# Kernel optimization log

Measured on AMD Instinct MI355X. Metric: run time of the kernel, lower is better.

The kernel has to match this reference:

```python
import jax, jax.numpy as jnp
import numpy as np

D_MODEL, N_HEAD, D_FF = 768, 12, 3072
HEAD_DIM = D_MODEL // N_HEAD
EPS = 1e-5


def _layernorm(x, g, b):
    mu = jnp.mean(x, axis=-1, keepdims=True)
    var = jnp.mean((x - mu) ** 2, axis=-1, keepdims=True)
    return (x - mu) * jax.lax.rsqrt(var + EPS) * g + b


def setup_inputs() -> dict:
    key = jax.random.key(0)
    ks = jax.random.split(key, 14)
    s = 1.0 / np.sqrt(D_MODEL)
    sf = 1.0 / np.sqrt(D_FF)
    inp = {
        "x": jax.random.normal(ks[0], (2, 2048, D_MODEL), dtype=jnp.float32),
        "Wq": jax.random.normal(ks[1], (D_MODEL, D_MODEL), dtype=jnp.float32) * s,
        "bq": jnp.zeros((D_MODEL,), jnp.float32),
        "Wk": jax.random.normal(ks[2], (D_MODEL, D_MODEL), dtype=jnp.float32) * s,
        "bk": jnp.zeros((D_MODEL,), jnp.float32),
        "Wv": jax.random.normal(ks[3], (D_MODEL, D_MODEL), dtype=jnp.float32) * s,
        "bv": jnp.zeros((D_MODEL,), jnp.float32),
        "Wo": jax.random.normal(ks[4], (D_MODEL, D_MODEL), dtype=jnp.float32) * s,
        "bo": jnp.zeros((D_MODEL,), jnp.float32),
        "W1": jax.random.normal(ks[5], (D_MODEL, D_FF), dtype=jnp.float32) * s,
        "b1": jnp.zeros((D_FF,), jnp.float32),
        "W2": jax.random.normal(ks[6], (D_FF, D_MODEL), dtype=jnp.float32) * sf,
        "b2": jnp.zeros((D_MODEL,), jnp.float32),
        "ln1_g": jnp.ones((D_MODEL,), jnp.float32),
        "ln1_b": jnp.zeros((D_MODEL,), jnp.float32),
        "ln2_g": jnp.ones((D_MODEL,), jnp.float32),
        "ln2_b": jnp.zeros((D_MODEL,), jnp.float32),
    }
    return inp


def reference(x, Wq, bq, Wk, bk, Wv, bv, Wo, bo, W1, b1, W2, b2,
              ln1_g, ln1_b, ln2_g, ln2_b):
    B, S, D = x.shape
    # projections -> [B, H, S, hd]
    def proj(W, b):
        return (x @ W + b).reshape(B, S, N_HEAD, HEAD_DIM).transpose(0, 2, 1, 3)
    q, k, v = proj(Wq, bq), proj(Wk, bk), proj(Wv, bv)
    scores = jnp.einsum("bhqd,bhkd->bhqk", q, k) / jnp.sqrt(
        jnp.asarray(HEAD_DIM, jnp.float32))
    attn = jax.nn.softmax(scores, axis=-1)
    ctx = jnp.einsum("bhqk,bhkd->bhqd", attn, v)
    ctx = ctx.transpose(0, 2, 1, 3).reshape(B, S, D)
    attn_out = ctx @ Wo + bo
    h = _layernorm(x + attn_out, ln1_g, ln1_b)
    ffn = jax.nn.gelu(h @ W1 + b1, approximate=False) @ W2 + b2
    return _layernorm(h + ffn, ln2_g, ln2_b)
```

## Files before the change

### kernel.cpp

```cpp
#include <hip/hip_runtime.h>
#include <hip/hip_bf16.h>
#include <cstdint>
#include <cstddef>

typedef unsigned short u16;
typedef __bf16 bf16x8 __attribute__((ext_vector_type(8)));
typedef float f32x4 __attribute__((ext_vector_type(4)));

#define MFMA_BF16(a, b, c) __builtin_amdgcn_mfma_f32_16x16x32_bf16((a), (b), (c), 0, 0, 0)

#define GLDS16(g, l)                                                        \
  __builtin_amdgcn_global_load_lds(                                         \
      (__attribute__((address_space(1))) void*)(void*)(g),                  \
      (__attribute__((address_space(3))) void*)(void*)(l), 16, 0, 0)

#define QSCALE 0.18033688011112042f

__device__ __forceinline__ u16 f2bf(float x) {
  union { float f; unsigned u; } c; c.f = x;
  unsigned u = c.u;
  unsigned r = (u + 0x7fffu + ((u >> 16) & 1u)) >> 16;
  return (u16)r;
}


__global__ __launch_bounds__(256) void transpose_bf16_k(
    const float* __restrict__ in, u16* __restrict__ out, int K, int N) {
  __shared__ float tile[32][33];
  const int tx = threadIdx.x & 31, ty = threadIdx.x >> 5;
  const int bx = blockIdx.x * 32;
  const int by = blockIdx.y * 32;
#pragma unroll
  for (int j = 0; j < 32; j += 8)
    tile[ty + j][tx] = in[(size_t)(by + ty + j) * N + bx + tx];
  __syncthreads();
#pragma unroll
  for (int j = 0; j < 32; j += 8)
    out[(size_t)(bx + ty + j) * K + by + tx] = f2bf(tile[tx][ty + j]);
}

__global__ __launch_bounds__(256) void cvt_bf16_k(
    const float* __restrict__ in, u16* __restrict__ out, int n) {
  int i = (blockIdx.x * 256 + threadIdx.x) * 4;
  if (i + 3 < n) {
    const float4 v = *(const float4*)(in + i);
    ushort4 o;
    o.x = f2bf(v.x); o.y = f2bf(v.y); o.z = f2bf(v.z); o.w = f2bf(v.w);
    *(ushort4*)(out + i) = o;
  }
}

__global__ __launch_bounds__(256) void concat3_k(
    const float* __restrict__ a, const float* __restrict__ b,
    const float* __restrict__ c, float* __restrict__ out) {
  int i = blockIdx.x * 256 + threadIdx.x;
  if (i < 768) out[i] = a[i];
  else if (i < 1536) out[i] = b[i - 768];
  else if (i < 2304) out[i] = c[i - 1536];
}

template <int EPI>
__global__ __launch_bounds__(256) void gemm_bt(
    const u16* __restrict__ A, const u16* __restrict__ BT,
    const float* __restrict__ bias, int M, int N, int K,
    float* __restrict__ outf, u16* __restrict__ outb,
    u16* __restrict__ qo, u16* __restrict__ ko, u16* __restrict__ vto) {
  __shared__ __align__(16) u16 lsA[128 * 32];
  __shared__ __align__(16) u16 lsB[128 * 32];
  const int tid = threadIdx.x;
  const int w = tid >> 6, lane = tid & 63;
  const int wm = w & 1, wn = w >> 1;
  const int lrow = lane & 15, quad = lane >> 4;
  const int m0 = blockIdx.y * 128, n0 = blockIdx.x * 128;

  f32x4 acc[4][4];
#pragma unroll
  for (int i = 0; i < 4; ++i)
#pragma unroll
    for (int j = 0; j < 4; ++j) acc[i][j] = (f32x4){0.f, 0.f, 0.f, 0.f};

  const int off = tid * 16;
  const int srow = off >> 6;
  const int scol = (off & 63) >> 1;

  for (int k0 = 0; k0 < K; k0 += 32) {
    const u16* ga = A + (size_t)(m0 + srow) * K + k0 + scol;
    const u16* gb = BT + (size_t)(n0 + srow) * K + k0 + scol;
    GLDS16(ga, (char*)lsA + off);
    GLDS16(ga + (size_t)64 * K, (char*)lsA + 4096 + off);
    GLDS16(gb, (char*)lsB + off);
    GLDS16(gb + (size_t)64 * K, (char*)lsB + 4096 + off);
    __syncthreads();
    bf16x8 af[4], bfr[4];
#pragma unroll
    for (int ms = 0; ms < 4; ++ms)
      af[ms] = *(const bf16x8*)&lsA[(wm * 64 + ms * 16 + lrow) * 32 + quad * 8];
#pragma unroll
    for (int ns = 0; ns < 4; ++ns)
      bfr[ns] = *(const bf16x8*)&lsB[(wn * 64 + ns * 16 + lrow) * 32 + quad * 8];
#pragma unroll
    for (int ms = 0; ms < 4; ++ms)
#pragma unroll
      for (int ns = 0; ns < 4; ++ns)
        acc[ms][ns] = MFMA_BF16(af[ms], bfr[ns], acc[ms][ns]);
    __syncthreads();
  }

#pragma unroll
  for (int ms = 0; ms < 4; ++ms) {
    const int rbase = m0 + wm * 64 + ms * 16 + quad * 4;
#pragma unroll
    for (int ns = 0; ns < 4; ++ns) {
      const int col = n0 + wn * 64 + ns * 16 + lrow;
      const float bcol = bias[col];
      if constexpr (EPI == 1) {
#pragma unroll
        for (int r = 0; r < 4; ++r)
          outf[(size_t)(rbase + r) * N + col] = acc[ms][ns][r] + bcol;
      } else if constexpr (EPI == 2) {
#pragma unroll
        for (int r = 0; r < 4; ++r) {
          float v = acc[ms][ns][r] + bcol;
          float g = 0.5f * v * (1.0f + erff(v * 0.7071067811865476f));
          outb[(size_t)(rbase + r) * N + col] = f2bf(g);
        }
      } else {
        const int which = col / 768;
        const int rem = col - which * 768;
        const int hh = rem >> 6, dd = rem & 63;
        const int bI = rbase >> 11, sI = rbase & 2047;
        const size_t bh = (size_t)bI * 12 + hh;
        if (which == 0) {
#pragma unroll
          for (int r = 0; r < 4; ++r)
            qo[(bh * 2048 + sI + r) * 64 + dd] = f2bf((acc[ms][ns][r] + bcol) * QSCALE);
        } else if (which == 1) {
#pragma unroll
          for (int r = 0; r < 4; ++r)
            ko[(bh * 2048 + sI + r) * 64 + dd] = f2bf(acc[ms][ns][r] + bcol);
        } else {
          ushort4 pk;
          pk.x = f2bf(acc[ms][ns][0] + bcol);
          pk.y = f2bf(acc[ms][ns][1] + bcol);
          pk.z = f2bf(acc[ms][ns][2] + bcol);
          pk.w = f2bf(acc[ms][ns][3] + bcol);
          *(ushort4*)(vto + (bh * 64 + dd) * 2048 + sI) = pk;
        }
      }
    }
  }
}

__global__ __launch_bounds__(256) void attn_kernel(
    const u16* __restrict__ q, const u16* __restrict__ k,
    const u16* __restrict__ vT, u16* __restrict__ ctx) {
  __shared__ __align__(16) u16 lsK[64 * 64];
  __shared__ __align__(16) u16 lsV[64 * 64];
  __shared__ __align__(16) u16 lsP[4][16 * 64];
  const int tid = threadIdx.x;
  const int w = tid >> 6, lane = tid & 63;
  const int lrow = lane & 15, quad = lane >> 4;
  const int bh = blockIdx.y;
  const int b = bh / 12, h = bh - b * 12;
  const int q0 = blockIdx.x * 64;

  const u16* qbase = q + (size_t)bh * 2048 * 64;
  const u16* kbase = k + (size_t)bh * 2048 * 64;
  const u16* vbase = vT + (size_t)bh * 64 * 2048;

  const int qrow = q0 + w * 16 + lrow;
  const bf16x8 qf0 = *(const bf16x8*)(qbase + (size_t)qrow * 64 + quad * 8);
  const bf16x8 qf1 = *(const bf16x8*)(qbase + (size_t)qrow * 64 + 32 + quad * 8);

  float lsum[4] = {0.f, 0.f, 0.f, 0.f};
  f32x4 oacc[4];
#pragma unroll
  for (int d = 0; d < 4; ++d) oacc[d] = (f32x4){0.f, 0.f, 0.f, 0.f};

  const int off = tid * 16;
  const int srow = off >> 7;
  const int schunk = (off >> 4) & 7;
  const int sxc = schunk ^ (srow & 7);
  const int ksrc = srow * 64 + sxc * 8;
  const int vsrc0 = srow * 2048 + sxc * 8;

  const int c0 = quad ^ (lrow & 7);
  const int rd0 = c0 * 8, rd1 = (c0 ^ 4) * 8;

  u16* const lsPw = &lsP[w][0];
  const int jhi_base = lrow >> 3, jlo = lrow & 7;

  for (int kt = 0; kt < 2048; kt += 64) {
    GLDS16(kbase + (size_t)kt * 64 + ksrc, (char*)lsK + off);
    GLDS16(kbase + (size_t)(kt + 32) * 64 + ksrc, (char*)lsK + 4096 + off);
    GLDS16(vbase + vsrc0 + kt, (char*)lsV + off);
    GLDS16(vbase + vsrc0 + kt + 32 * 2048, (char*)lsV + 4096 + off);
    __syncthreads();

    f32x4 sc[4];
#pragma unroll
    for (int ns = 0; ns < 4; ++ns) {
      sc[ns] = (f32x4){0.f, 0.f, 0.f, 0.f};
      const u16* kr = &lsK[(ns * 16 + lrow) * 64];
      bf16x8 kf0 = *(const bf16x8*)(kr + rd0);
      bf16x8 kf1 = *(const bf16x8*)(kr + rd1);
      sc[ns] = MFMA_BF16(qf0, kf0, sc[ns]);
      sc[ns] = MFMA_BF16(qf1, kf1, sc[ns]);
    }

#pragma unroll
    for (int ns = 0; ns < 4; ++ns) {
      const int jhi = ns * 2 + jhi_base;
#pragma unroll
      for (int r = 0; r < 4; ++r) {
        float p = __builtin_amdgcn_exp2f(sc[ns][r]);
        lsum[r] += p;
        union { float f; unsigned u; } cv; cv.f = p;
        const int m = quad * 4 + r;
        lsPw[m * 64 + ((jhi ^ (m & 7)) * 8) + jlo] = (u16)(cv.u >> 16);
      }
    }

    const u16* pr = lsPw + lrow * 64;
    const bf16x8 pf0 = *(const bf16x8*)(pr + rd0);
    const bf16x8 pf1 = *(const bf16x8*)(pr + rd1);
#pragma unroll
    for (int d = 0; d < 4; ++d) {
      const u16* vr = &lsV[(d * 16 + lrow) * 64];
      bf16x8 vf0 = *(const bf16x8*)(vr + rd0);
      bf16x8 vf1 = *(const bf16x8*)(vr + rd1);
      oacc[d] = MFMA_BF16(pf0, vf0, oacc[d]);
      oacc[d] = MFMA_BF16(pf1, vf1, oacc[d]);
    }
    __syncthreads();
  }

#pragma unroll
  for (int r = 0; r < 4; ++r) {
#pragma unroll
    for (int mm = 1; mm <= 8; mm <<= 1) lsum[r] += __shfl_xor(lsum[r], mm);
  }
  float invl[4];
#pragma unroll
  for (int r = 0; r < 4; ++r) invl[r] = 1.f / lsum[r];

  const int srow_out = q0 + w * 16 + quad * 4;
#pragma unroll
  for (int d = 0; d < 4; ++d)
#pragma unroll
    for (int r = 0; r < 4; ++r)
      ctx[(size_t)(b * 2048 + srow_out + r) * 768 + h * 64 + d * 16 + lrow] =
          f2bf(oacc[d][r] * invl[r]);
}

__global__ __launch_bounds__(256) void ln_kernel(
    const float* __restrict__ a, const float* __restrict__ res,
    const float* __restrict__ g, const float* __restrict__ bb,
    float* __restrict__ outf, u16* __restrict__ outb) {
  const int row = blockIdx.x;
  const int tid = threadIdx.x;
  const float* pa = a + (size_t)row * 768;
  const float* pr = res + (size_t)row * 768;
  float v[3], s = 0.f, s2 = 0.f;
#pragma unroll
  for (int j = 0; j < 3; ++j) {
    float t = pa[tid + j * 256] + pr[tid + j * 256];
    v[j] = t; s += t; s2 += t * t;
  }
#pragma unroll
  for (int m = 32; m > 0; m >>= 1) {
    s += __shfl_xor(s, m);
    s2 += __shfl_xor(s2, m);
  }
  __shared__ float red[8];
  const int w = tid >> 6, lane = tid & 63;
  if (lane == 0) { red[w] = s; red[4 + w] = s2; }
  __syncthreads();
  s = red[0] + red[1] + red[2] + red[3];
  s2 = red[4] + red[5] + red[6] + red[7];
  const float mu = s * (1.f / 768.f);
  const float var = s2 * (1.f / 768.f) - mu * mu;
  const float rstd = rsqrtf(var + 1e-5f);
#pragma unroll
  for (int j = 0; j < 3; ++j) {
    const int c = tid + j * 256;
    const float y = (v[j] - mu) * rstd * g[c] + bb[c];
    if (outf) outf[(size_t)row * 768 + c] = y;
    if (outb) outb[(size_t)row * 768 + c] = f2bf(y);
  }
}

extern "C" void kernel_launch(void* const* d_in, const int* in_sizes, int n_in,
                              void* d_out, int out_size, void* d_ws, size_t ws_size,
                              hipStream_t stream) {
  const float* x    = (const float*)d_in[0];
  const float* Wq   = (const float*)d_in[1];
  const float* bq   = (const float*)d_in[2];
  const float* Wk   = (const float*)d_in[3];
  const float* bk   = (const float*)d_in[4];
  const float* Wv   = (const float*)d_in[5];
  const float* bv   = (const float*)d_in[6];
  const float* Wo   = (const float*)d_in[7];
  const float* bo   = (const float*)d_in[8];
  const float* W1   = (const float*)d_in[9];
  const float* b1   = (const float*)d_in[10];
  const float* W2   = (const float*)d_in[11];
  const float* b2   = (const float*)d_in[12];
  const float* ln1g = (const float*)d_in[13];
  const float* ln1b = (const float*)d_in[14];
  const float* ln2g = (const float*)d_in[15];
  const float* ln2b = (const float*)d_in[16];

  char* ws = (char*)d_ws;
  size_t off = 0;
  auto alloc = [&](size_t bytes) {
    void* p = ws + off;
    off += (bytes + 255) & ~(size_t)255;
    return p;
  };
  u16*  WqkvT = (u16*)alloc(2304ull * 768 * 2);
  u16*  WoT   = (u16*)alloc(768ull * 768 * 2);
  u16*  W1T   = (u16*)alloc(3072ull * 768 * 2);
  u16*  W2T   = (u16*)alloc(768ull * 3072 * 2);
  float* bqkv = (float*)alloc(2304 * 4);
  u16*  xb    = (u16*)alloc(4096ull * 768 * 2);
  u16*  qb    = (u16*)alloc(24ull * 2048 * 64 * 2);
  u16*  kb    = (u16*)alloc(24ull * 2048 * 64 * 2);
  u16*  vtb   = (u16*)alloc(24ull * 64 * 2048 * 2);
  u16*  ctx   = (u16*)alloc(4096ull * 768 * 2);
  float* attno = (float*)alloc(4096ull * 768 * 4);
  float* hbuf  = (float*)alloc(4096ull * 768 * 4);
  u16*  hb    = (u16*)alloc(4096ull * 768 * 2);
  u16*  f1    = (u16*)alloc(4096ull * 3072 * 2);
  float* f2b  = (float*)alloc(4096ull * 768 * 4);

  transpose_bf16_k<<<dim3(24, 24), 256, 0, stream>>>(Wq, WqkvT, 768, 768);
  transpose_bf16_k<<<dim3(24, 24), 256, 0, stream>>>(Wk, WqkvT + 768 * 768, 768, 768);
  transpose_bf16_k<<<dim3(24, 24), 256, 0, stream>>>(Wv, WqkvT + 2 * 768 * 768, 768, 768);
  transpose_bf16_k<<<dim3(24, 24), 256, 0, stream>>>(Wo, WoT, 768, 768);
  transpose_bf16_k<<<dim3(96, 24), 256, 0, stream>>>(W1, W1T, 768, 3072);
  transpose_bf16_k<<<dim3(24, 96), 256, 0, stream>>>(W2, W2T, 3072, 768);
  concat3_k<<<9, 256, 0, stream>>>(bq, bk, bv, bqkv);
  cvt_bf16_k<<<3072, 256, 0, stream>>>(x, xb, 4096 * 768);

  gemm_bt<0><<<dim3(18, 32), 256, 0, stream>>>(xb, WqkvT, bqkv, 4096, 2304, 768,
                                               nullptr, nullptr, qb, kb, vtb);
  attn_kernel<<<dim3(32, 24), 256, 0, stream>>>(qb, kb, vtb, ctx);
  gemm_bt<1><<<dim3(6, 32), 256, 0, stream>>>(ctx, WoT, bo, 4096, 768, 768,
                                              attno, nullptr, nullptr, nullptr, nullptr);
  ln_kernel<<<4096, 256, 0, stream>>>(x, attno, ln1g, ln1b, hbuf, hb);
  gemm_bt<2><<<dim3(24, 32), 256, 0, stream>>>(hb, W1T, b1, 4096, 3072, 768,
                                               nullptr, f1, nullptr, nullptr, nullptr);
  gemm_bt<1><<<dim3(6, 32), 256, 0, stream>>>(f1, W2T, b2, 4096, 768, 3072,
                                              f2b, nullptr, nullptr, nullptr, nullptr);
  ln_kernel<<<4096, 256, 0, stream>>>(hbuf, f2b, ln2g, ln2b, (float*)d_out, nullptr);
}
```

Baseline: 357.7 us.

## Split-K narrow GEMMs with partial sums reduced in layernorm, widen K tile with swizzle

The GEMM K-step doubles from 32 to 64 and the LDS layout gets an XOR swizzle to cut bank conflicts. The two N=768 GEMMs (output projection and FFN down-projection) now split K across blockIdx.z (2 and 4 ways) so more workgroups fill the GPU. They write fp32 partial sums that the layernorm kernel adds together along with the bias. f2b reuses the workspace region that starts at xb, which means attention-phase buffers get overwritten. This costs extra partial-sum memory traffic and LDS use.

```diff
diff --git a/kernel.cpp b/kernel.cpp
--- a/kernel.cpp
+++ b/kernel.cpp
@@ -15,6 +15,7 @@
       (__attribute__((address_space(3))) void*)(void*)(l), 16, 0, 0)
 
 #define QSCALE 0.18033688011112042f
+#define PSTRIDE ((size_t)4096 * 768)
 
 __device__ __forceinline__ u16 f2bf(float x) {
   union { float f; unsigned u; } c; c.f = x;
@@ -62,16 +63,17 @@
 template <int EPI>
 __global__ __launch_bounds__(256) void gemm_bt(
     const u16* __restrict__ A, const u16* __restrict__ BT,
-    const float* __restrict__ bias, int M, int N, int K,
+    const float* __restrict__ bias, int M, int N, int K, int kchunk,
     float* __restrict__ outf, u16* __restrict__ outb,
     u16* __restrict__ qo, u16* __restrict__ ko, u16* __restrict__ vto) {
-  __shared__ __align__(16) u16 lsA[128 * 32];
-  __shared__ __align__(16) u16 lsB[128 * 32];
+  __shared__ __align__(16) u16 lsA[128 * 64];
+  __shared__ __align__(16) u16 lsB[128 * 64];
   const int tid = threadIdx.x;
   const int w = tid >> 6, lane = tid & 63;
   const int wm = w & 1, wn = w >> 1;
   const int lrow = lane & 15, quad = lane >> 4;
   const int m0 = blockIdx.y * 128, n0 = blockIdx.x * 128;
+  const int kbeg = blockIdx.z * kchunk, kend = kbeg + kchunk;
 
   f32x4 acc[4][4];
 #pragma unroll
@@ -80,44 +82,54 @@
     for (int j = 0; j < 4; ++j) acc[i][j] = (f32x4){0.f, 0.f, 0.f, 0.f};
 
   const int off = tid * 16;
-  const int srow = off >> 6;
-  const int scol = (off & 63) >> 1;
-
-  for (int k0 = 0; k0 < K; k0 += 32) {
+  const int srow = off >> 7;
+  const int schunk = (off >> 4) & 7;
+  const int sxc = schunk ^ (srow & 7);
+  const int scol = sxc * 8;
+
+  const int rsw = lrow & 7;
+
+  for (int k0 = kbeg; k0 < kend; k0 += 64) {
     const u16* ga = A + (size_t)(m0 + srow) * K + k0 + scol;
     const u16* gb = BT + (size_t)(n0 + srow) * K + k0 + scol;
-    GLDS16(ga, (char*)lsA + off);
-    GLDS16(ga + (size_t)64 * K, (char*)lsA + 4096 + off);
-    GLDS16(gb, (char*)lsB + off);
-    GLDS16(gb + (size_t)64 * K, (char*)lsB + 4096 + off);
+#pragma unroll
+    for (int c = 0; c < 4; ++c) {
+      GLDS16(ga + (size_t)(c * 32) * K, (char*)lsA + c * 4096 + off);
+      GLDS16(gb + (size_t)(c * 32) * K, (char*)lsB + c * 4096 + off);
+    }
     __syncthreads();
-    bf16x8 af[4], bfr[4];
-#pragma unroll
-    for (int ms = 0; ms < 4; ++ms)
-      af[ms] = *(const bf16x8*)&lsA[(wm * 64 + ms * 16 + lrow) * 32 + quad * 8];
-#pragma unroll
-    for (int ns = 0; ns < 4; ++ns)
-      bfr[ns] = *(const bf16x8*)&lsB[(wn * 64 + ns * 16 + lrow) * 32 + quad * 8];
-#pragma unroll
-    for (int ms = 0; ms < 4; ++ms)
+#pragma unroll
+    for (int ks = 0; ks < 2; ++ks) {
+      const int slot = ((ks * 4 + quad) ^ rsw) * 8;
+      bf16x8 af[4], bfr[4];
+#pragma unroll
+      for (int ms = 0; ms < 4; ++ms)
+        af[ms] = *(const bf16x8*)&lsA[(wm * 64 + ms * 16 + lrow) * 64 + slot];
 #pragma unroll
       for (int ns = 0; ns < 4; ++ns)
-        acc[ms][ns] = MFMA_BF16(af[ms], bfr[ns], acc[ms][ns]);
+        bfr[ns] = *(const bf16x8*)&lsB[(wn * 64 + ns * 16 + lrow) * 64 + slot];
+#pragma unroll
+      for (int ms = 0; ms < 4; ++ms)
+#pragma unroll
+        for (int ns = 0; ns < 4; ++ns)
+          acc[ms][ns] = MFMA_BF16(af[ms], bfr[ns], acc[ms][ns]);
+    }
     __syncthreads();
   }
 
+  float* const pf = (EPI == 3) ? outf + (size_t)blockIdx.z * M * N : outf;
 #pragma unroll
   for (int ms = 0; ms < 4; ++ms) {
     const int rbase = m0 + wm * 64 + ms * 16 + quad * 4;
 #pragma unroll
     for (int ns = 0; ns < 4; ++ns) {
       const int col = n0 + wn * 64 + ns * 16 + lrow;
-      const float bcol = bias[col];
-      if constexpr (EPI == 1) {
+      if constexpr (EPI == 3) {
 #pragma unroll
         for (int r = 0; r < 4; ++r)
-          outf[(size_t)(rbase + r) * N + col] = acc[ms][ns][r] + bcol;
+          pf[(size_t)(rbase + r) * N + col] = acc[ms][ns][r];
       } else if constexpr (EPI == 2) {
+        const float bcol = bias[col];
 #pragma unroll
         for (int r = 0; r < 4; ++r) {
           float v = acc[ms][ns][r] + bcol;
@@ -125,6 +137,7 @@
           outb[(size_t)(rbase + r) * N + col] = f2bf(g);
         }
       } else {
+        const float bcol = bias[col];
         const int which = col / 768;
         const int rem = col - which * 768;
         const int hh = rem >> 6, dd = rem & 63;
@@ -254,17 +267,19 @@
 }
 
 __global__ __launch_bounds__(256) void ln_kernel(
-    const float* __restrict__ a, const float* __restrict__ res,
-    const float* __restrict__ g, const float* __restrict__ bb,
-    float* __restrict__ outf, u16* __restrict__ outb) {
+    const float* __restrict__ parts, int nparts, const float* __restrict__ bias,
+    const float* __restrict__ res, const float* __restrict__ g,
+    const float* __restrict__ bb, float* __restrict__ outf, u16* __restrict__ outb) {
   const int row = blockIdx.x;
   const int tid = threadIdx.x;
-  const float* pa = a + (size_t)row * 768;
   const float* pr = res + (size_t)row * 768;
   float v[3], s = 0.f, s2 = 0.f;
 #pragma unroll
   for (int j = 0; j < 3; ++j) {
-    float t = pa[tid + j * 256] + pr[tid + j * 256];
+    const int c = tid + j * 256;
+    float t = bias[c] + pr[c];
+    for (int p = 0; p < nparts; ++p)
+      t += parts[p * PSTRIDE + (size_t)row * 768 + c];
     v[j] = t; s += t; s2 += t * t;
   }
 #pragma unroll
@@ -323,16 +338,17 @@
   u16*  W1T   = (u16*)alloc(3072ull * 768 * 2);
   u16*  W2T   = (u16*)alloc(768ull * 3072 * 2);
   float* bqkv = (float*)alloc(2304 * 4);
+  char* bigbase = (char*)alloc(0);
   u16*  xb    = (u16*)alloc(4096ull * 768 * 2);
   u16*  qb    = (u16*)alloc(24ull * 2048 * 64 * 2);
   u16*  kb    = (u16*)alloc(24ull * 2048 * 64 * 2);
   u16*  vtb   = (u16*)alloc(24ull * 64 * 2048 * 2);
   u16*  ctx   = (u16*)alloc(4096ull * 768 * 2);
-  float* attno = (float*)alloc(4096ull * 768 * 4);
+  float* attno = (float*)alloc(2ull * PSTRIDE * 4);
+  float* f2b   = (float*)bigbase;
   float* hbuf  = (float*)alloc(4096ull * 768 * 4);
   u16*  hb    = (u16*)alloc(4096ull * 768 * 2);
   u16*  f1    = (u16*)alloc(4096ull * 3072 * 2);
-  float* f2b  = (float*)alloc(4096ull * 768 * 4);
 
   transpose_bf16_k<<<dim3(24, 24), 256, 0, stream>>>(Wq, WqkvT, 768, 768);
   transpose_bf16_k<<<dim3(24, 24), 256, 0, stream>>>(Wk, WqkvT + 768 * 768, 768, 768);
@@ -343,15 +359,15 @@
   concat3_k<<<9, 256, 0, stream>>>(bq, bk, bv, bqkv);
   cvt_bf16_k<<<3072, 256, 0, stream>>>(x, xb, 4096 * 768);
 
-  gemm_bt<0><<<dim3(18, 32), 256, 0, stream>>>(xb, WqkvT, bqkv, 4096, 2304, 768,
-                                               nullptr, nullptr, qb, kb, vtb);
+  gemm_bt<0><<<dim3(18, 32, 1), 256, 0, stream>>>(xb, WqkvT, bqkv, 4096, 2304, 768, 768,
+                                                  nullptr, nullptr, qb, kb, vtb);
   attn_kernel<<<dim3(32, 24), 256, 0, stream>>>(qb, kb, vtb, ctx);
-  gemm_bt<1><<<dim3(6, 32), 256, 0, stream>>>(ctx, WoT, bo, 4096, 768, 768,
-                                              attno, nullptr, nullptr, nullptr, nullptr);
-  ln_kernel<<<4096, 256, 0, stream>>>(x, attno, ln1g, ln1b, hbuf, hb);
-  gemm_bt<2><<<dim3(24, 32), 256, 0, stream>>>(hb, W1T, b1, 4096, 3072, 768,
-                                               nullptr, f1, nullptr, nullptr, nullptr);
-  gemm_bt<1><<<dim3(6, 32), 256, 0, stream>>>(f1, W2T, b2, 4096, 768, 3072,
-                                              f2b, nullptr, nullptr, nullptr, nullptr);
-  ln_kernel<<<4096, 256, 0, stream>>>(hbuf, f2b, ln2g, ln2b, (float*)d_out, nullptr);
-}
+  gemm_bt<3><<<dim3(6, 32, 2), 256, 0, stream>>>(ctx, WoT, nullptr, 4096, 768, 768, 384,
+                                                 attno, nullptr, nullptr, nullptr, nullptr);
+  ln_kernel<<<4096, 256, 0, stream>>>(attno, 2, bo, x, ln1g, ln1b, hbuf, hb);
+  gemm_bt<2><<<dim3(24, 32, 1), 256, 0, stream>>>(hb, W1T, b1, 4096, 3072, 768, 768,
+                                                  nullptr, f1, nullptr, nullptr, nullptr);
+  gemm_bt<3><<<dim3(6, 32, 4), 256, 0, stream>>>(f1, W2T, nullptr, 4096, 768, 3072, 768,
+                                                 f2b, nullptr, nullptr, nullptr, nullptr);
+  ln_kernel<<<4096, 256, 0, stream>>>(f2b, 4, b2, hbuf, ln2g, ln2b, (float*)d_out, nullptr);
+}
```

Result: faster. 312.2 us (-12.7%).
